# Kernel tuning notes

Hardware: AMD Instinct MI355X
Metric: run time of the kernel (lower is better)

Reference implementation:

```python
import jax, jax.numpy as jnp
import numpy as np
from jax import lax

K = 16      # neighbors per point (module init arg)
B = 16      # number of point clouds (equal-sized, per batch ids)
P = 4096    # points per cloud


def setup_inputs() -> dict:
    key = jax.random.key(0)
    x = jax.random.normal(key, (B * P, 3), dtype=jnp.float32)
    batch = jnp.repeat(jnp.arange(B, dtype=jnp.int64), P)  # sorted, equal-sized clouds
    return {"x": x, "batch": batch}


def _knn_indices(xb):
    # xb: (B, P, 3). Squared pairwise distances via |a|^2 + |b|^2 - 2 a.b
    sq = jnp.sum(xb * xb, axis=-1)                      # (B, P)
    d = sq[:, :, None] + sq[:, None, :] - 2.0 * jnp.einsum('bpc,bqc->bpq', xb, xb)
    # knn_graph(loop=False): exclude self-edges
    eye = jnp.eye(P, dtype=bool)
    d = jnp.where(eye[None], jnp.inf, d)                # (B, P, P)
    _, idx = lax.top_k(-d, K)                            # (B, P, K) nearest neighbors
    return idx


def reference(x, batch):
    # batch ids are sorted with equal cloud sizes -> dense per-cloud layout
    xb = x.reshape(B, P, 3)
    idx = _knn_indices(xb)                               # (B, P, K)
    neighbors = jax.vmap(lambda pts, ind: pts[ind])(xb, idx)  # (B, P, K, 3)
    mean = neighbors.mean(axis=2, keepdims=True)         # (B, P, 1, 3)
    c = neighbors - mean
    cov = jnp.einsum('bpki,bpkj->bpij', c, c) / K        # (B, P, 3, 3)
    out = jnp.concatenate([xb, cov.reshape(B, P, 9)], axis=-1)
    return out.reshape(B * P, 12)
```

## Files before the change

### kernel.cpp

```cpp
#include <hip/hip_runtime.h>

#define PTS    4096
#define TPB    256
#define PPB    64
#define QTR    1024
#define NSUB   64
#define CAP    36
#define NCLOUD 16
#define UMAX   0xFFFFFFFFu

template<int N>
__device__ __forceinline__ void insN(unsigned key, unsigned (&s)[N], unsigned &cmax) {
  if (key < cmax) {
    bool done = false;
#pragma unroll
    for (int i = 0; i < N; ++i) {
      bool c = (!done) && (s[i] == cmax);
      s[i] = c ? key : s[i];
      done = done || c;
    }
    cmax = s[0];
#pragma unroll
    for (int i = 1; i < N; ++i) cmax = (s[i] > cmax) ? s[i] : cmax;
  }
}

__global__ __launch_bounds__(TPB, 4) void knn_cov(const float* __restrict__ x,
                                                  float* __restrict__ out) {
  __shared__ unsigned scol[CAP * TPB];
  __shared__ unsigned scnt[TPB];

  const int tid  = threadIdx.x;
  const int lane = tid & 63;
  const int h     = __builtin_amdgcn_readfirstlane(tid >> 6);
  const int cloud = blockIdx.x >> 6;
  const int chunk = blockIdx.x & 63;
  const int p     = chunk * PPB + lane;

  const float* __restrict__ xc = x + (size_t)cloud * PTS * 3;

  const float px = xc[p * 3 + 0];
  const float py = xc[p * 3 + 1];
  const float pz = xc[p * 3 + 2];

  const int c0 = h * QTR;
  const float* __restrict__ cc = xc + (size_t)c0 * 3;

  float m[NSUB];
#pragma unroll
  for (int j = 0; j < NSUB; ++j) m[j] = 3.4e38f;
  for (int t0 = 0; t0 < QTR; t0 += NSUB) {
#pragma unroll
    for (int g = 0; g < NSUB / 8; ++g) {
#pragma unroll
      for (int j = 0; j < 8; ++j) {
        const int ci = t0 + g * 8 + j;
        const float qx = cc[ci * 3 + 0];
        const float qy = cc[ci * 3 + 1];
        const float qz = cc[ci * 3 + 2];
        const float dx = qx - px, dy = qy - py, dz = qz - pz;
        const float d  = fmaf(dz, dz, fmaf(dy, dy, dx * dx));
        const int mi   = g * 8 + j;
        m[mi] = fminf(m[mi], d);
      }
    }
  }

  unsigned s17[17], cm;
#pragma unroll
  for (int j = 0; j < 17; ++j) s17[j] = __float_as_uint(m[j]);
  cm = s17[0];
#pragma unroll
  for (int j = 1; j < 17; ++j) cm = (s17[j] > cm) ? s17[j] : cm;
#pragma unroll
  for (int j = 17; j < NSUB; ++j) insN<17>(__float_as_uint(m[j]), s17, cm);
  const float Tval = __uint_as_float(cm);

  unsigned cnt = 0;
  for (int t0 = 0; t0 < QTR; t0 += 8) {
#pragma unroll
    for (int j = 0; j < 8; ++j) {
      const int ci = t0 + j;
      const float qx = cc[ci * 3 + 0];
      const float qy = cc[ci * 3 + 1];
      const float qz = cc[ci * 3 + 2];
      const float dx = qx - px, dy = qy - py, dz = qz - pz;
      const float d  = fmaf(dz, dz, fmaf(dy, dy, dx * dx));
      if (d <= Tval) {
        const unsigned slot = (cnt < (unsigned)CAP) ? cnt : (unsigned)(CAP - 1);
        scol[slot * TPB + tid] =
            (__float_as_uint(d) & 0xFFFFF000u) | (unsigned)(c0 + ci);
        cnt++;
      }
    }
  }

  if (cnt > (unsigned)CAP) {
    unsigned sf[17], cmf = UMAX;
#pragma unroll
    for (int j = 0; j < 17; ++j) sf[j] = UMAX;
#pragma unroll 4
    for (int ci = 0; ci < QTR; ++ci) {
      const float qx = cc[ci * 3 + 0];
      const float qy = cc[ci * 3 + 1];
      const float qz = cc[ci * 3 + 2];
      const float dx = qx - px, dy = qy - py, dz = qz - pz;
      const float d  = fmaf(dz, dz, fmaf(dy, dy, dx * dx));
      const unsigned kb = (__float_as_uint(d) & 0xFFFFF000u) | (unsigned)(c0 + ci);
      insN<17>(kb, sf, cmf);
    }
#pragma unroll
    for (int j = 0; j < 17; ++j) scol[j * TPB + tid] = sf[j];
    cnt = 17;
  }
  scnt[tid] = cnt;
  __syncthreads();

  if (tid < PPB) {
    unsigned s16[16], cm16 = UMAX;
#pragma unroll
    for (int j = 0; j < 16; ++j) s16[j] = UMAX;
    const unsigned selfk = (unsigned)p;
#pragma unroll
    for (int k = 0; k < 4; ++k) {
      const int col = k * PPB + tid;
      const unsigned n = scnt[col];
      unsigned w = n;
#pragma unroll
      for (int off = 32; off >= 1; off >>= 1) {
        unsigned o = (unsigned)__shfl_xor((int)w, off, 64);
        w = (o > w) ? o : w;
      }
      for (unsigned j = 0; j < w; ++j) {
        unsigned kb = (j < n) ? scol[j * TPB + col] : UMAX;
        kb = (kb == selfk) ? UMAX : kb;
        insN<16>(kb, s16, cm16);
      }
    }

    float Sx = 0, Sy = 0, Sz = 0;
    float Sxx = 0, Sxy = 0, Sxz = 0, Syy = 0, Syz = 0, Szz = 0;
#pragma unroll
    for (int j = 0; j < 16; ++j) {
      const int idx = (int)(s16[j] & 0xFFFu);
      const float nx = xc[idx * 3 + 0];
      const float ny = xc[idx * 3 + 1];
      const float nz = xc[idx * 3 + 2];
      Sx += nx; Sy += ny; Sz += nz;
      Sxx = fmaf(nx, nx, Sxx); Sxy = fmaf(nx, ny, Sxy); Sxz = fmaf(nx, nz, Sxz);
      Syy = fmaf(ny, ny, Syy); Syz = fmaf(ny, nz, Syz); Szz = fmaf(nz, nz, Szz);
    }
    const float sc = 0.0625f;
    const float mx = Sx * sc, my = Sy * sc, mz = Sz * sc;
    const float cxx = fmaf(-mx, mx, Sxx * sc);
    const float cxy = fmaf(-mx, my, Sxy * sc);
    const float cxz = fmaf(-mx, mz, Sxz * sc);
    const float cyy = fmaf(-my, my, Syy * sc);
    const float cyz = fmaf(-my, mz, Syz * sc);
    const float czz = fmaf(-mz, mz, Szz * sc);

    const int gid = cloud * PTS + p;
    float4* o4 = (float4*)(out + (size_t)gid * 12);
    o4[0] = make_float4(px, py, pz, cxx);
    o4[1] = make_float4(cxy, cxz, cxy, cyy);
    o4[2] = make_float4(cyz, cxz, cyz, czz);
  }
}

extern "C" void kernel_launch(void* const* d_in, const int* in_sizes, int n_in,
                              void* d_out, int out_size, void* d_ws, size_t ws_size,
                              hipStream_t stream) {
  const float* x = (const float*)d_in[0];
  float* out = (float*)d_out;
  dim3 grid(NCLOUD * (PTS / PPB));
  knn_cov<<<grid, TPB, 0, stream>>>(x, out);
}
```

Before: 201.8 us.

## Pack points to SoA in workspace and vectorize distance passes with float2

Adds a pre-pass kernel that transposes the xyz points into a structure-of-arrays layout in the workspace. The main kernel then loads candidates as float2 pairs and computes two distances at a time, which may map to packed FP32 instructions. The running-minimum bucket count drops from 64 to 32 to save registers. This costs an extra launch and a full read/write of the point array, and fewer buckets give a looser threshold, so more candidates can pass and the overflow path may run more often. The original AoS kernel is kept as a fallback when the workspace is too small.

Result: slower. 308.0 us (+52.6%).

```diff
diff --git a/kernel.cpp b/kernel.cpp
--- a/kernel.cpp
+++ b/kernel.cpp
@@ -4,10 +4,13 @@
 #define TPB    256
 #define PPB    64
 #define QTR    1024
-#define NSUB   64
+#define NSUB   32
 #define CAP    36
 #define NCLOUD 16
+#define NTOT   (NCLOUD * PTS)
 #define UMAX   0xFFFFFFFFu
+
+typedef __attribute__((ext_vector_type(2))) float f32x2;
 
 template<int N>
 __device__ __forceinline__ void insN(unsigned key, unsigned (&s)[N], unsigned &cmax) {
@@ -25,71 +28,89 @@
   }
 }
 
-__global__ __launch_bounds__(TPB, 4) void knn_cov(const float* __restrict__ x,
-                                                  float* __restrict__ out) {
+__global__ void soa_pack(const float* __restrict__ x, float* __restrict__ ws) {
+  const int g = blockIdx.x * TPB + threadIdx.x;
+  ws[g]            = x[3 * g + 0];
+  ws[NTOT + g]     = x[3 * g + 1];
+  ws[2 * NTOT + g] = x[3 * g + 2];
+}
+
+__global__ __launch_bounds__(TPB, 4) void knn_cov_soa(const float* __restrict__ ws,
+                                                      float* __restrict__ out) {
   __shared__ unsigned scol[CAP * TPB];
   __shared__ unsigned scnt[TPB];
 
-  const int tid  = threadIdx.x;
-  const int lane = tid & 63;
+  const int tid   = threadIdx.x;
+  const int lane  = tid & 63;
   const int h     = __builtin_amdgcn_readfirstlane(tid >> 6);
   const int cloud = blockIdx.x >> 6;
   const int chunk = blockIdx.x & 63;
   const int p     = chunk * PPB + lane;
 
-  const float* __restrict__ xc = x + (size_t)cloud * PTS * 3;
-
-  const float px = xc[p * 3 + 0];
-  const float py = xc[p * 3 + 1];
-  const float pz = xc[p * 3 + 2];
+  const float* __restrict__ Xs = ws + (size_t)cloud * PTS;
+  const float* __restrict__ Ys = Xs + NTOT;
+  const float* __restrict__ Zs = Xs + 2 * NTOT;
+
+  const float px = Xs[p], py = Ys[p], pz = Zs[p];
+  f32x2 vx; vx.x = px; vx.y = px;
+  f32x2 vy; vy.x = py; vy.y = py;
+  f32x2 vz; vz.x = pz; vz.y = pz;
 
   const int c0 = h * QTR;
-  const float* __restrict__ cc = xc + (size_t)c0 * 3;
-
-  float m[NSUB];
-#pragma unroll
-  for (int j = 0; j < NSUB; ++j) m[j] = 3.4e38f;
+  const float* __restrict__ qx = Xs + c0;
+  const float* __restrict__ qy = Ys + c0;
+  const float* __restrict__ qz = Zs + c0;
+
+  f32x2 m2[16];
+#pragma unroll
+  for (int j = 0; j < 16; ++j) { m2[j].x = 3.4e38f; m2[j].y = 3.4e38f; }
   for (int t0 = 0; t0 < QTR; t0 += NSUB) {
 #pragma unroll
-    for (int g = 0; g < NSUB / 8; ++g) {
-#pragma unroll
-      for (int j = 0; j < 8; ++j) {
-        const int ci = t0 + g * 8 + j;
-        const float qx = cc[ci * 3 + 0];
-        const float qy = cc[ci * 3 + 1];
-        const float qz = cc[ci * 3 + 2];
-        const float dx = qx - px, dy = qy - py, dz = qz - pz;
-        const float d  = fmaf(dz, dz, fmaf(dy, dy, dx * dx));
-        const int mi   = g * 8 + j;
-        m[mi] = fminf(m[mi], d);
-      }
-    }
-  }
-
+    for (int j = 0; j < 16; ++j) {
+      const int i2 = (t0 >> 1) + j;
+      const f32x2 ax = *(const f32x2*)(qx + 2 * i2);
+      const f32x2 ay = *(const f32x2*)(qy + 2 * i2);
+      const f32x2 az = *(const f32x2*)(qz + 2 * i2);
+      const f32x2 dx = ax - vx, dy = ay - vy, dz = az - vz;
+      const f32x2 d  = dx * dx + dy * dy + dz * dz;
+      m2[j].x = fminf(m2[j].x, d.x);
+      m2[j].y = fminf(m2[j].y, d.y);
+    }
+  }
+
+  float mm[32];
+#pragma unroll
+  for (int j = 0; j < 16; ++j) { mm[2 * j] = m2[j].x; mm[2 * j + 1] = m2[j].y; }
   unsigned s17[17], cm;
 #pragma unroll
-  for (int j = 0; j < 17; ++j) s17[j] = __float_as_uint(m[j]);
+  for (int j = 0; j < 17; ++j) s17[j] = __float_as_uint(mm[j]);
   cm = s17[0];
 #pragma unroll
   for (int j = 1; j < 17; ++j) cm = (s17[j] > cm) ? s17[j] : cm;
 #pragma unroll
-  for (int j = 17; j < NSUB; ++j) insN<17>(__float_as_uint(m[j]), s17, cm);
+  for (int j = 17; j < NSUB; ++j) insN<17>(__float_as_uint(mm[j]), s17, cm);
   const float Tval = __uint_as_float(cm);
 
   unsigned cnt = 0;
-  for (int t0 = 0; t0 < QTR; t0 += 8) {
+  for (int t0 = 0; t0 < QTR; t0 += 16) {
 #pragma unroll
     for (int j = 0; j < 8; ++j) {
-      const int ci = t0 + j;
-      const float qx = cc[ci * 3 + 0];
-      const float qy = cc[ci * 3 + 1];
-      const float qz = cc[ci * 3 + 2];
-      const float dx = qx - px, dy = qy - py, dz = qz - pz;
-      const float d  = fmaf(dz, dz, fmaf(dy, dy, dx * dx));
-      if (d <= Tval) {
+      const int i2 = (t0 >> 1) + j;
+      const f32x2 ax = *(const f32x2*)(qx + 2 * i2);
+      const f32x2 ay = *(const f32x2*)(qy + 2 * i2);
+      const f32x2 az = *(const f32x2*)(qz + 2 * i2);
+      const f32x2 dx = ax - vx, dy = ay - vy, dz = az - vz;
+      const f32x2 d  = dx * dx + dy * dy + dz * dz;
+      if (d.x <= Tval) {
         const unsigned slot = (cnt < (unsigned)CAP) ? cnt : (unsigned)(CAP - 1);
         scol[slot * TPB + tid] =
-            (__float_as_uint(d) & 0xFFFFF000u) | (unsigned)(c0 + ci);
+            (__float_as_uint(d.x) & 0xFFFFF000u) | (unsigned)(c0 + 2 * i2);
+        cnt++;
+      }
+      if (d.y <= Tval) {
+        const unsigned slot = (cnt < (unsigned)CAP) ? cnt : (unsigned)(CAP - 1);
+        scol[slot * TPB + tid] =
+            (__float_as_uint(d.y) & 0xFFFFF000u) | (unsigned)(c0 + 2 * i2 + 1);
         cnt++;
       }
     }
@@ -101,13 +122,9 @@
     for (int j = 0; j < 17; ++j) sf[j] = UMAX;
 #pragma unroll 4
     for (int ci = 0; ci < QTR; ++ci) {
-      const float qx = cc[ci * 3 + 0];
-      const float qy = cc[ci * 3 + 1];
-      const float qz = cc[ci * 3 + 2];
-      const float dx = qx - px, dy = qy - py, dz = qz - pz;
+      const float dx = qx[ci] - px, dy = qy[ci] - py, dz = qz[ci] - pz;
       const float d  = fmaf(dz, dz, fmaf(dy, dy, dx * dx));
-      const unsigned kb = (__float_as_uint(d) & 0xFFFFF000u) | (unsigned)(c0 + ci);
-      insN<17>(kb, sf, cmf);
+      insN<17>((__float_as_uint(d) & 0xFFFFF000u) | (unsigned)(c0 + ci), sf, cmf);
     }
 #pragma unroll
     for (int j = 0; j < 17; ++j) scol[j * TPB + tid] = sf[j];
@@ -143,9 +160,7 @@
 #pragma unroll
     for (int j = 0; j < 16; ++j) {
       const int idx = (int)(s16[j] & 0xFFFu);
-      const float nx = xc[idx * 3 + 0];
-      const float ny = xc[idx * 3 + 1];
-      const float nz = xc[idx * 3 + 2];
+      const float nx = Xs[idx], ny = Ys[idx], nz = Zs[idx];
       Sx += nx; Sy += ny; Sz += nz;
       Sxx = fmaf(nx, nx, Sxx); Sxy = fmaf(nx, ny, Sxy); Sxz = fmaf(nx, nz, Sxz);
       Syy = fmaf(ny, ny, Syy); Syz = fmaf(ny, nz, Syz); Szz = fmaf(nz, nz, Szz);
@@ -167,11 +182,139 @@
   }
 }
 
+__global__ __launch_bounds__(TPB, 4) void knn_cov_aos(const float* __restrict__ x,
+                                                      float* __restrict__ out) {
+  __shared__ unsigned scol[CAP * TPB];
+  __shared__ unsigned scnt[TPB];
+
+  const int tid   = threadIdx.x;
+  const int lane  = tid & 63;
+  const int h     = __builtin_amdgcn_readfirstlane(tid >> 6);
+  const int cloud = blockIdx.x >> 6;
+  const int chunk = blockIdx.x & 63;
+  const int p     = chunk * PPB + lane;
+
+  const float* __restrict__ xc = x + (size_t)cloud * PTS * 3;
+  const float px = xc[p * 3 + 0], py = xc[p * 3 + 1], pz = xc[p * 3 + 2];
+  const int c0 = h * QTR;
+  const float* __restrict__ cc = xc + (size_t)c0 * 3;
+
+  float m[NSUB];
+#pragma unroll
+  for (int j = 0; j < NSUB; ++j) m[j] = 3.4e38f;
+  for (int t0 = 0; t0 < QTR; t0 += NSUB) {
+#pragma unroll
+    for (int j = 0; j < NSUB; ++j) {
+      const int ci = t0 + j;
+      const float dx = cc[ci * 3 + 0] - px, dy = cc[ci * 3 + 1] - py,
+                  dz = cc[ci * 3 + 2] - pz;
+      const float d = fmaf(dz, dz, fmaf(dy, dy, dx * dx));
+      m[j] = fminf(m[j], d);
+    }
+  }
+  unsigned s17[17], cm;
+#pragma unroll
+  for (int j = 0; j < 17; ++j) s17[j] = __float_as_uint(m[j]);
+  cm = s17[0];
+#pragma unroll
+  for (int j = 1; j < 17; ++j) cm = (s17[j] > cm) ? s17[j] : cm;
+#pragma unroll
+  for (int j = 17; j < NSUB; ++j) insN<17>(__float_as_uint(m[j]), s17, cm);
+  const float Tval = __uint_as_float(cm);
+
+  unsigned cnt = 0;
+  for (int t0 = 0; t0 < QTR; t0 += 8) {
+#pragma unroll
+    for (int j = 0; j < 8; ++j) {
+      const int ci = t0 + j;
+      const float dx = cc[ci * 3 + 0] - px, dy = cc[ci * 3 + 1] - py,
+                  dz = cc[ci * 3 + 2] - pz;
+      const float d = fmaf(dz, dz, fmaf(dy, dy, dx * dx));
+      if (d <= Tval) {
+        const unsigned slot = (cnt < (unsigned)CAP) ? cnt : (unsigned)(CAP - 1);
+        scol[slot * TPB + tid] =
+            (__float_as_uint(d) & 0xFFFFF000u) | (unsigned)(c0 + ci);
+        cnt++;
+      }
+    }
+  }
+  if (cnt > (unsigned)CAP) {
+    unsigned sf[17], cmf = UMAX;
+#pragma unroll
+    for (int j = 0; j < 17; ++j) sf[j] = UMAX;
+#pragma unroll 4
+    for (int ci = 0; ci < QTR; ++ci) {
+      const float dx = cc[ci * 3 + 0] - px, dy = cc[ci * 3 + 1] - py,
+                  dz = cc[ci * 3 + 2] - pz;
+      const float d = fmaf(dz, dz, fmaf(dy, dy, dx * dx));
+      insN<17>((__float_as_uint(d) & 0xFFFFF000u) | (unsigned)(c0 + ci), sf, cmf);
+    }
+#pragma unroll
+    for (int j = 0; j < 17; ++j) scol[j * TPB + tid] = sf[j];
+    cnt = 17;
+  }
+  scnt[tid] = cnt;
+  __syncthreads();
+
+  if (tid < PPB) {
+    unsigned s16[16], cm16 = UMAX;
+#pragma unroll
+    for (int j = 0; j < 16; ++j) s16[j] = UMAX;
+    const unsigned selfk = (unsigned)p;
+#pragma unroll
+    for (int k = 0; k < 4; ++k) {
+      const int col = k * PPB + tid;
+      const unsigned n = scnt[col];
+      unsigned w = n;
+#pragma unroll
+      for (int off = 32; off >= 1; off >>= 1) {
+        unsigned o = (unsigned)__shfl_xor((int)w, off, 64);
+        w = (o > w) ? o : w;
+      }
+      for (unsigned j = 0; j < w; ++j) {
+        unsigned kb = (j < n) ? scol[j * TPB + col] : UMAX;
+        kb = (kb == selfk) ? UMAX : kb;
+        insN<16>(kb, s16, cm16);
+      }
+    }
+    float Sx = 0, Sy = 0, Sz = 0;
+    float Sxx = 0, Sxy = 0, Sxz = 0, Syy = 0, Syz = 0, Szz = 0;
+#pragma unroll
+    for (int j = 0; j < 16; ++j) {
+      const int idx = (int)(s16[j] & 0xFFFu);
+      const float nx = xc[idx * 3 + 0], ny = xc[idx * 3 + 1], nz = xc[idx * 3 + 2];
+      Sx += nx; Sy += ny; Sz += nz;
+      Sxx = fmaf(nx, nx, Sxx); Sxy = fmaf(nx, ny, Sxy); Sxz = fmaf(nx, nz, Sxz);
+      Syy = fmaf(ny, ny, Syy); Syz = fmaf(ny, nz, Syz); Szz = fmaf(nz, nz, Szz);
+    }
+    const float sc = 0.0625f;
+    const float mx = Sx * sc, my = Sy * sc, mz = Sz * sc;
+    const float cxx = fmaf(-mx, mx, Sxx * sc);
+    const float cxy = fmaf(-mx, my, Sxy * sc);
+    const float cxz = fmaf(-mx, mz, Sxz * sc);
+    const float cyy = fmaf(-my, my, Syy * sc);
+    const float cyz = fmaf(-my, mz, Syz * sc);
+    const float czz = fmaf(-mz, mz, Szz * sc);
+
+    const int gid = cloud * PTS + p;
+    float4* o4 = (float4*)(out + (size_t)gid * 12);
+    o4[0] = make_float4(px, py, pz, cxx);
+    o4[1] = make_float4(cxy, cxz, cxy, cyy);
+    o4[2] = make_float4(cyz, cxz, cyz, czz);
+  }
+}
+
 extern "C" void kernel_launch(void* const* d_in, const int* in_sizes, int n_in,
                               void* d_out, int out_size, void* d_ws, size_t ws_size,
                               hipStream_t stream) {
   const float* x = (const float*)d_in[0];
   float* out = (float*)d_out;
   dim3 grid(NCLOUD * (PTS / PPB));
-  knn_cov<<<grid, TPB, 0, stream>>>(x, out);
-}
+  if (ws_size >= (size_t)3 * NTOT * sizeof(float)) {
+    float* ws = (float*)d_ws;
+    soa_pack<<<NTOT / TPB, TPB, 0, stream>>>(x, ws);
+    knn_cov_soa<<<grid, TPB, 0, stream>>>(ws, out);
+  } else {
+    knn_cov_aos<<<grid, TPB, 0, stream>>>(x, out);
+  }
+}
```
